# Kernel optimization log

Hardware: AMD Instinct MI355X
Metric: run time of the kernel (lower is better)

## Reference

```python
import jax, jax.numpy as jnp
from jax import lax
import numpy as np

B = 4096

def _conv(x, w, b):
    # x: [B,C,H,W], w: [O,I,3,3] torch OIHW layout, VALID, stride 1
    y = lax.conv_general_dilated(x, w, (1, 1), 'VALID',
                                 dimension_numbers=('NCHW', 'OIHW', 'NCHW'))
    return y + b[None, :, None, None]

def _pool2(x):
    return lax.reduce_window(x, -jnp.inf, lax.max, (1, 1, 2, 2), (1, 1, 2, 2), 'VALID')

def _lin(x, w, b):
    # torch Linear: y = x @ W^T + b, W: [out, in]
    return x @ w.T + b

def setup_inputs() -> dict:
    key = jax.random.key(0)
    ks = jax.random.split(key, 24)
    def w(k, shape, fan_in):
        return (jax.random.normal(k, shape, dtype=jnp.float32) / np.sqrt(fan_in)).astype(jnp.float32)
    inp = {
        'x':      jax.random.normal(ks[0], (B, 1, 28, 28), dtype=jnp.float32),
        'c1_w':   w(ks[1], (50, 1, 3, 3), 9),      'c1_b':  jnp.zeros((50,), jnp.float32),
        'c2_w':   w(ks[2], (50, 50, 3, 3), 450),   'c2_b':  jnp.zeros((50,), jnp.float32),
        'c3_w':   w(ks[3], (50, 50, 3, 3), 450),   'c3_b':  jnp.zeros((50,), jnp.float32),
        'l1c1_w': w(ks[4], (500, 50 * 13 * 13), 50 * 13 * 13), 'l1c1_b': jnp.zeros((500,), jnp.float32),
        'l2c1_w': w(ks[5], (10, 500), 500),        'l2c1_b': jnp.zeros((10,), jnp.float32),
        'l1c2_w': w(ks[6], (500, 50 * 5 * 5), 50 * 5 * 5),     'l1c2_b': jnp.zeros((500,), jnp.float32),
        'l2c2_w': w(ks[7], (10, 500), 500),        'l2c2_b': jnp.zeros((10,), jnp.float32),
        'l1_w':   w(ks[8], (500, 50), 50),         'l1_b':  jnp.zeros((500,), jnp.float32),
        'l2_w':   w(ks[9], (10, 500), 500),        'l2_b':  jnp.zeros((10,), jnp.float32),
        'd1_w':   w(ks[10], (2, 50 * 13 * 13), 50 * 13 * 13),  'd1_b':  jnp.zeros((2,), jnp.float32),
        'd2_w':   w(ks[11], (2, 50 * 5 * 5), 50 * 5 * 5),      'd2_b':  jnp.zeros((2,), jnp.float32),
    }
    return inp

def reference(x, c1_w, c1_b, c2_w, c2_b, c3_w, c3_b,
              l1c1_w, l1c1_b, l2c1_w, l2c1_b,
              l1c2_w, l1c2_b, l2c2_w, l2c2_b,
              l1_w, l1_b, l2_w, l2_b, d1_w, d1_b, d2_w, d2_b):
    b = x.shape[0]
    # stage 1
    h1 = _pool2(jax.nn.relu(_conv(x, c1_w, c1_b)))           # [B,50,13,13]
    f1 = h1.reshape(b, 50 * 13 * 13)
    exit1 = jnp.argmax(_lin(f1, d1_w, d1_b), axis=1) == 0     # [B] bool
    out1 = _lin(_lin(f1, l1c1_w, l1c1_b), l2c1_w, l2c1_b)     # [B,10] (no relu, as in source)
    # stage 2 (computed densely; selection below replicates the gather/scatter routing)
    h2 = _pool2(jax.nn.relu(_conv(h1, c2_w, c2_b)))          # [B,50,5,5]
    f2 = h2.reshape(b, 50 * 5 * 5)
    exit2 = jnp.argmax(_lin(f2, d2_w, d2_b), axis=1) == 0
    out2 = _lin(_lin(f2, l1c2_w, l1c2_b), l2c2_w, l2c2_b)
    # stage 3
    h3 = _pool2(jax.nn.relu(_conv(h2, c3_w, c3_b)))          # [B,50,1,1]
    f3 = h3.reshape(b, 50)
    out3 = _lin(jax.nn.relu(_lin(f3, l1_w, l1_b)), l2_w, l2_b)
    sel = jnp.where(exit1[:, None], out1, jnp.where(exit2[:, None], out2, out3))
    # original returns cat(out1_subset, out2_subset, out3_subset) + an index order;
    # we return the equivalent per-sample outputs in original batch order.
    return jax.nn.log_softmax(sel, axis=1)
```

## Files before the change

### kernel.cpp

```cpp
#include <hip/hip_runtime.h>
#include <hip/hip_bf16.h>
#include <cstdint>


typedef __bf16 bf16_t;
typedef __bf16 bf16x8 __attribute__((ext_vector_type(8)));
typedef float  f32x4  __attribute__((ext_vector_type(4)));

#define B_IMG 4096


__device__ void role_conv1(char* smem, int blk,
    const float* __restrict__ x, const float* __restrict__ w1,
    const float* __restrict__ b1, float* __restrict__ h1)
{
    float* ws = (float*)smem;
    float* bs = ws + 456;
    const int t = threadIdx.x;
    for (int i = t; i < 450; i += 256) ws[i] = w1[i];
    if (t < 50) bs[t] = b1[t];
    __syncthreads();

    const int idx = blk * 256 + t;
    if (idx >= B_IMG * 169) return;
    const int b   = idx / 169;
    const int pos = idx % 169;
    const int py = pos / 13, px = pos % 13;

    const float* xp = x + (size_t)b * 784 + (2 * py) * 28 + 2 * px;
    float p[4][4];
#pragma unroll
    for (int r = 0; r < 4; ++r)
#pragma unroll
        for (int c = 0; c < 4; ++c) p[r][c] = xp[r * 28 + c];

    float* hb = h1 + (size_t)b * 8480 + pos;
    if (pos < 30) h1[(size_t)b * 8480 + 8450 + pos] = 0.f;

    for (int oc = 0; oc < 50; ++oc) {
        const float* wp = &ws[oc * 9];
        const float w00 = wp[0], w01 = wp[1], w02 = wp[2];
        const float w10 = wp[3], w11 = wp[4], w12 = wp[5];
        const float w20 = wp[6], w21 = wp[7], w22 = wp[8];
        float a[2][2];
#pragma unroll
        for (int dy = 0; dy < 2; ++dy)
#pragma unroll
            for (int dx = 0; dx < 2; ++dx) {
                a[dy][dx] = p[dy + 0][dx + 0] * w00 + p[dy + 0][dx + 1] * w01 + p[dy + 0][dx + 2] * w02
                          + p[dy + 1][dx + 0] * w10 + p[dy + 1][dx + 1] * w11 + p[dy + 1][dx + 2] * w12
                          + p[dy + 2][dx + 0] * w20 + p[dy + 2][dx + 1] * w21 + p[dy + 2][dx + 2] * w22;
            }
        float v = fmaxf(fmaxf(a[0][0], a[0][1]), fmaxf(a[1][0], a[1][1])) + bs[oc];
        hb[oc * 169] = fmaxf(v, 0.f);
    }
}

__device__ void role_wb16(int blk, const float* __restrict__ src,
                          bf16_t* __restrict__ dst, int N, int K, int Kp, int total)
{
    const int idx = blk * 256 + threadIdx.x;
    if (idx >= total) return;
    const int n = idx / Kp, k = idx % Kp;
    const float v = (n < N && k < K) ? src[(size_t)n * K + k] : 0.f;
    dst[idx] = (bf16_t)v;
}

__device__ void role_w2t(int blk, const float* __restrict__ w2, float* __restrict__ w2p)
{
    const int idx = blk * 256 + threadIdx.x;
    if (idx >= 50 * 600) return;
    const int ic = idx / 600, r = idx % 600, oc = r / 12, j = r % 12;
    w2p[idx] = (j < 9) ? w2[oc * 450 + ic * 9 + j] : 0.f;
}

__device__ void role_conv2(char* smem, int b,
    const float* __restrict__ h1, const float* __restrict__ w2p,
    const float* __restrict__ b2, float* __restrict__ h2)
{
    float* in   = (float*)smem;
    float* wbuf = in + 1360;
    const int t = threadIdx.x;

    for (int s = t; s < 676; s += 256) in[s] = h1[(size_t)b * 8480 + s];
    {
        const float4* src = (const float4*)w2p;
        float4* dst = (float4*)wbuf;
        for (int s = t; s < 600; s += 256) dst[s] = src[s];
    }
    __syncthreads();
    if (t < 30) h2[(size_t)b * 1280 + 1250 + t] = 0.f;

    const int ocg = t / 25;
    const int pos = t % 25;
    const int py = pos / 5, px = pos % 5;
    const int oc0 = ocg * 5;
    const bool act = (t < 250);

    float acc[5][4];
#pragma unroll
    for (int j = 0; j < 5; ++j)
#pragma unroll
        for (int q = 0; q < 4; ++q) acc[j][q] = 0.f;

    for (int ic0 = 0; ic0 < 50; ic0 += 4) {
        const int cur = (ic0 >> 2) & 1;
        if (ic0 + 4 < 50) {
            const int nxt = cur ^ 1;
            const int nic2 = (50 - ic0 - 4 < 4) ? (50 - ic0 - 4) : 4;
            for (int s = t; s < nic2 * 169; s += 256)
                in[nxt * 680 + s] = h1[(size_t)b * 8480 + (ic0 + 4) * 169 + s];
            const float4* src = (const float4*)(w2p + (size_t)(ic0 + 4) * 600);
            float4* dst = (float4*)(wbuf + nxt * 2400);
            for (int s = t; s < nic2 * 150; s += 256) dst[s] = src[s];
        }
        if (act) {
            const int nic = (50 - ic0 < 4) ? (50 - ic0) : 4;
            const float* ibc = in + cur * 680 + (2 * py) * 13 + 2 * px;
            for (int icl = 0; icl < nic; ++icl) {
                float p[4][4];
                const float* ip = ibc + icl * 169;
#pragma unroll
                for (int r = 0; r < 4; ++r)
#pragma unroll
                    for (int c = 0; c < 4; ++c) p[r][c] = ip[r * 13 + c];
                const float* wl = wbuf + cur * 2400 + icl * 600 + oc0 * 12;
#pragma unroll
                for (int j = 0; j < 5; ++j) {
                    const f32x4 wv0 = *(const f32x4*)(wl + j * 12);
                    const f32x4 wv1 = *(const f32x4*)(wl + j * 12 + 4);
                    const f32x4 wv2 = *(const f32x4*)(wl + j * 12 + 8);
                    const float w00 = wv0[0], w01 = wv0[1], w02 = wv0[2];
                    const float w10 = wv0[3], w11 = wv1[0], w12 = wv1[1];
                    const float w20 = wv1[2], w21 = wv1[3], w22 = wv2[0];
#pragma unroll
                    for (int dy = 0; dy < 2; ++dy)
#pragma unroll
                        for (int dx = 0; dx < 2; ++dx) {
                            acc[j][dy * 2 + dx] +=
                                  p[dy + 0][dx + 0] * w00 + p[dy + 0][dx + 1] * w01 + p[dy + 0][dx + 2] * w02
                                + p[dy + 1][dx + 0] * w10 + p[dy + 1][dx + 1] * w11 + p[dy + 1][dx + 2] * w12
                                + p[dy + 2][dx + 0] * w20 + p[dy + 2][dx + 1] * w21 + p[dy + 2][dx + 2] * w22;
                        }
                }
            }
        }
        __syncthreads();
    }

    if (act) {
#pragma unroll
        for (int j = 0; j < 5; ++j) {
            float v = fmaxf(fmaxf(acc[j][0], acc[j][1]), fmaxf(acc[j][2], acc[j][3]));
            h2[(size_t)b * 1280 + (oc0 + j) * 25 + pos] = fmaxf(v + b2[oc0 + j], 0.f);
        }
    }
}

__device__ void role_conv3(char* smem, int blk,
    const float* __restrict__ h2, const float* __restrict__ w3,
    const float* __restrict__ b3, float* __restrict__ f3)
{
    float* in = (float*)smem;
    const int t = threadIdx.x;
    for (int i = t; i < 5000; i += 256) {
        const int img = i / 1250, off = i % 1250;
        in[i] = h2[(size_t)(blk * 4 + img) * 1280 + off];
    }
    __syncthreads();
    const int il = t >> 6;
    const int oc = t & 63;
    if (oc >= 50) return;

    const float* ip0 = &in[il * 1250];
    float a00 = 0.f, a01 = 0.f, a10 = 0.f, a11 = 0.f;
    for (int ic = 0; ic < 50; ++ic) {
        float p[4][4];
        const float* ip = ip0 + ic * 25;
#pragma unroll
        for (int r = 0; r < 4; ++r)
#pragma unroll
            for (int c = 0; c < 4; ++c) p[r][c] = ip[r * 5 + c];
        const float* wp = &w3[((size_t)oc * 50 + ic) * 9];
        const float w00 = wp[0], w01 = wp[1], w02 = wp[2];
        const float w10 = wp[3], w11 = wp[4], w12 = wp[5];
        const float w20 = wp[6], w21 = wp[7], w22 = wp[8];
        a00 += p[0][0]*w00 + p[0][1]*w01 + p[0][2]*w02 + p[1][0]*w10 + p[1][1]*w11 + p[1][2]*w12 + p[2][0]*w20 + p[2][1]*w21 + p[2][2]*w22;
        a01 += p[0][1]*w00 + p[0][2]*w01 + p[0][3]*w02 + p[1][1]*w10 + p[1][2]*w11 + p[1][3]*w12 + p[2][1]*w20 + p[2][2]*w21 + p[2][3]*w22;
        a10 += p[1][0]*w00 + p[1][1]*w01 + p[1][2]*w02 + p[2][0]*w10 + p[2][1]*w11 + p[2][2]*w12 + p[3][0]*w20 + p[3][1]*w21 + p[3][2]*w22;
        a11 += p[1][1]*w00 + p[1][2]*w01 + p[1][3]*w02 + p[2][1]*w10 + p[2][2]*w11 + p[2][3]*w12 + p[3][1]*w20 + p[3][2]*w21 + p[3][3]*w22;
    }
    float v = fmaxf(fmaxf(a00, a01), fmaxf(a10, a11)) + b3[oc];
    f3[(size_t)(blk * 4 + il) * 50 + oc] = fmaxf(v, 0.f);
}

__device__ void role_exit(char* smem, int b,
    const float* __restrict__ F, int ldf, int K,
    const float* __restrict__ dw, const float* __restrict__ db, int* __restrict__ e)
{
    float* r0 = (float*)smem;
    float* r1 = r0 + 256;
    const int t = threadIdx.x;
    const float* f = F + (size_t)b * ldf;
    float s0 = 0.f, s1 = 0.f;
    for (int i = t; i < K; i += 256) {
        const float v = f[i];
        s0 += v * dw[i];
        s1 += v * dw[K + i];
    }
    r0[t] = s0; r1[t] = s1;
    __syncthreads();
    for (int s = 128; s > 0; s >>= 1) {
        if (t < s) { r0[t] += r0[t + s]; r1[t] += r1[t + s]; }
        __syncthreads();
    }
    if (t == 0) e[b] = (r0[0] + db[0] >= r1[0] + db[1]) ? 1 : 0;
}

__device__ void role_gemm(char* smem, int g,
    const float* __restrict__ A, int lda, const bf16_t* __restrict__ W,
    const float* __restrict__ bias, float* __restrict__ C0, float* __restrict__ C1,
    int Kp, int khalf, int Nout, int ldc)
{
    bf16_t* As = (bf16_t*)smem;
    bf16_t* Bs = As + 128 * 40;

    const int t = threadIdx.x;
    const int m0 = (g & 31) * 128;
    const int n0 = ((g >> 5) & 7) * 64;
    const int kz = g >> 8;
    const int kbeg = kz ? khalf : 0;
    const int kend = kz ? Kp : khalf;
    float* C = kz ? C1 : C0;

    const int wave = t >> 6;
    const int lane = t & 63;
    const int wm = (wave >> 1) * 64;
    const int wn = (wave & 1) * 32;
    const int quad = lane >> 4;
    const int lr = lane & 15;

    f32x4 acc[4][2];
#pragma unroll
    for (int i = 0; i < 4; ++i)
#pragma unroll
        for (int j = 0; j < 2; ++j) acc[i][j] = (f32x4)0.f;

    const int ar = t >> 2;
    const int ac = (t & 3) * 8;

    for (int k0 = kbeg; k0 < kend; k0 += 32) {
        __syncthreads();
#pragma unroll
        for (int h = 0; h < 2; ++h) {
            const float* ap = A + (size_t)(m0 + ar + h * 64) * lda + k0 + ac;
            const float4 f0 = *(const float4*)ap;
            const float4 f1 = *(const float4*)(ap + 4);
            bf16x8 v;
            v[0] = (bf16_t)f0.x; v[1] = (bf16_t)f0.y; v[2] = (bf16_t)f0.z; v[3] = (bf16_t)f0.w;
            v[4] = (bf16_t)f1.x; v[5] = (bf16_t)f1.y; v[6] = (bf16_t)f1.z; v[7] = (bf16_t)f1.w;
            *(bf16x8*)&As[(ar + h * 64) * 40 + ac] = v;
        }
        *(uint4*)&Bs[ar * 40 + ac] = *(const uint4*)&W[(size_t)(n0 + ar) * Kp + k0 + ac];
        __syncthreads();

        bf16x8 af[4], bfr[2];
#pragma unroll
        for (int i = 0; i < 4; ++i)
            af[i] = *(const bf16x8*)&As[(wm + i * 16 + lr) * 40 + quad * 8];
#pragma unroll
        for (int j = 0; j < 2; ++j)
            bfr[j] = *(const bf16x8*)&Bs[(wn + j * 16 + lr) * 40 + quad * 8];
#pragma unroll
        for (int i = 0; i < 4; ++i)
#pragma unroll
            for (int j = 0; j < 2; ++j)
                acc[i][j] = __builtin_amdgcn_mfma_f32_16x16x32_bf16(af[i], bfr[j], acc[i][j], 0, 0, 0);
    }

#pragma unroll
    for (int j = 0; j < 2; ++j) {
        const int n = n0 + wn + j * 16 + lr;
        const float bv = (kz == 0 && n < Nout) ? bias[n] : 0.f;
#pragma unroll
        for (int i = 0; i < 4; ++i) {
            const int mrow = m0 + wm + i * 16 + quad * 4;
#pragma unroll
            for (int r = 0; r < 4; ++r)
                C[(size_t)(mrow + r) * ldc + n] = acc[i][j][r] + bv;
        }
    }
}

__device__ void role_lin10(char* smem, int blk,
    const float* __restrict__ U, const float* __restrict__ U2, int ldu,
    const float* __restrict__ W, const float* __restrict__ bias,
    float* __restrict__ out)
{
    float* red = (float*)smem;
    const int t = threadIdx.x;
    const int ks = t & 15;
    const int il = t >> 4;
    const int b  = blk * 16 + il;
    const float* u = U + (size_t)b * ldu;

    float acc[10];
#pragma unroll
    for (int o = 0; o < 10; ++o) acc[o] = 0.f;

    if (U2) {
        const float* u2 = U2 + (size_t)b * ldu;
        for (int i = 0; i < 31; ++i) {
            const int k = ks + i * 16;
            const float uv = u[k] + u2[k];
#pragma unroll
            for (int o = 0; o < 10; ++o) acc[o] += uv * W[o * 500 + k];
        }
        const int k = ks + 496;
        if (k < 500) {
            const float uv = u[k] + u2[k];
#pragma unroll
            for (int o = 0; o < 10; ++o) acc[o] += uv * W[o * 500 + k];
        }
    } else {
        for (int i = 0; i < 31; ++i) {
            const int k = ks + i * 16;
            const float uv = u[k];
#pragma unroll
            for (int o = 0; o < 10; ++o) acc[o] += uv * W[o * 500 + k];
        }
        const int k = ks + 496;
        if (k < 500) {
            const float uv = u[k];
#pragma unroll
            for (int o = 0; o < 10; ++o) acc[o] += uv * W[o * 500 + k];
        }
    }
#pragma unroll
    for (int o = 0; o < 10; ++o) red[(il * 10 + o) * 17 + ks] = acc[o];
    __syncthreads();
    if (t < 160) {
        const int il2 = t / 10, o = t - il2 * 10;
        float s = 0.f;
#pragma unroll
        for (int q = 0; q < 16; ++q) s += red[(il2 * 10 + o) * 17 + q];
        out[(size_t)(blk * 16 + il2) * 10 + o] = s + bias[o];
    }
}


__global__ __launch_bounds__(256) void k_prep(
    const float* x, const float* c1w, const float* c1b, float* h1,
    const float* l1c1w, bf16_t* Wb1, const float* l1c2w, bf16_t* Wb2,
    const float* c2w, float* w2p)
{
    extern __shared__ char smem[];
    const int g = blockIdx.x;
    if (g < 2704)        role_conv1(smem, g, x, c1w, c1b, h1);
    else if (g < 19664)  role_wb16(g - 2704, l1c1w, Wb1, 500, 8450, 8480, 512 * 8480);
    else if (g < 22224)  role_wb16(g - 19664, l1c2w, Wb2, 500, 1250, 1280, 512 * 1280);
    else                 role_w2t(g - 22224, c2w, w2p);
}

__global__ __launch_bounds__(256) void k_stage1(
    const float* h1, const bf16_t* Wb1, const float* l1c1b, float* u, float* up,
    const float* d1w, const float* d1b, int* e1,
    const float* w2p, const float* c2b, float* h2)
{
    extern __shared__ char smem[];
    const int g = blockIdx.x;
    if (g < 512)         role_gemm(smem, g, h1, 8480, Wb1, l1c1b, u, up, 8480, 4256, 500, 512);
    else if (g < 4608)   role_conv2(smem, g - 512, h1, w2p, c2b, h2);
    else                 role_exit(smem, g - 4608, h1, 8480, 8450, d1w, d1b, e1);
}

__global__ __launch_bounds__(256) void k_stage2(
    const float* h2, const bf16_t* Wb2, const float* l1c2b, float* v, float* vp,
    const float* d2w, const float* d2b, int* e2,
    const float* c3w, const float* c3b, float* f3,
    const float* u, const float* up, const float* l2c1w, const float* l2c1b, float* out1)
{
    extern __shared__ char smem[];
    const int g = blockIdx.x;
    if (g < 512)         role_gemm(smem, g, h2, 1280, Wb2, l1c2b, v, vp, 1280, 640, 500, 512);
    else if (g < 1536)   role_conv3(smem, g - 512, h2, c3w, c3b, f3);
    else if (g < 1792)   role_lin10(smem, g - 1536, u, up, 512, l2c1w, l2c1b, out1);
    else                 role_exit(smem, g - 1792, h2, 1280, 1250, d2w, d2b, e2);
}

__global__ __launch_bounds__(256) void k_tail(
    const float* __restrict__ v, const float* __restrict__ vp,
    const float* __restrict__ l2c2w, const float* __restrict__ l2c2b,
    const float* __restrict__ f3, const float* __restrict__ l1w, const float* __restrict__ l1b,
    const float* __restrict__ l2w, const float* __restrict__ l2b,
    const float* __restrict__ out1, const int* __restrict__ e1, const int* __restrict__ e2,
    float* __restrict__ out)
{
    __shared__ float fs[800];
    __shared__ float u3loc[8000];
    __shared__ float red[2720];
    __shared__ float o2loc[160];
    __shared__ float o3loc[160];

    const int t   = threadIdx.x;
    const int blk = blockIdx.x;
    const int ks  = t & 15;
    const int il  = t >> 4;

    for (int i = t; i < 800; i += 256) fs[i] = f3[(size_t)blk * 800 + i];
    __syncthreads();

    for (int im = 0; im < 16; ++im) {
        for (int o = t; o < 500; o += 256) {
            float s = 0.f;
#pragma unroll
            for (int k = 0; k < 50; ++k) s += fs[im * 50 + k] * l1w[o * 50 + k];
            u3loc[im * 500 + o] = fmaxf(s + l1b[o], 0.f);
        }
    }

    {
        const float* uu  = v  + (size_t)(blk * 16 + il) * 512;
        const float* uu2 = vp + (size_t)(blk * 16 + il) * 512;
        float acc[10];
#pragma unroll
        for (int o = 0; o < 10; ++o) acc[o] = 0.f;
        for (int i = 0; i < 31; ++i) {
            const int k = ks + i * 16;
            const float uv = uu[k] + uu2[k];
#pragma unroll
            for (int o = 0; o < 10; ++o) acc[o] += uv * l2c2w[o * 500 + k];
        }
        const int k = ks + 496;
        if (k < 500) {
            const float uv = uu[k] + uu2[k];
#pragma unroll
            for (int o = 0; o < 10; ++o) acc[o] += uv * l2c2w[o * 500 + k];
        }
        __syncthreads();
#pragma unroll
        for (int o = 0; o < 10; ++o) red[(il * 10 + o) * 17 + ks] = acc[o];
        __syncthreads();
        if (t < 160) {
            const int il2 = t / 10, o = t - il2 * 10;
            float s = 0.f;
#pragma unroll
            for (int q = 0; q < 16; ++q) s += red[(il2 * 10 + o) * 17 + q];
            o2loc[t] = s + l2c2b[o];
        }
        __syncthreads();
    }

    {
        const float* uu = u3loc + il * 500;
        float acc[10];
#pragma unroll
        for (int o = 0; o < 10; ++o) acc[o] = 0.f;
        for (int i = 0; i < 31; ++i) {
            const int k = ks + i * 16;
            const float uv = uu[k];
#pragma unroll
            for (int o = 0; o < 10; ++o) acc[o] += uv * l2w[o * 500 + k];
        }
        const int k = ks + 496;
        if (k < 500) {
            const float uv = uu[k];
#pragma unroll
            for (int o = 0; o < 10; ++o) acc[o] += uv * l2w[o * 500 + k];
        }
#pragma unroll
        for (int o = 0; o < 10; ++o) red[(il * 10 + o) * 17 + ks] = acc[o];
        __syncthreads();
        if (t < 160) {
            const int il2 = t / 10, o = t - il2 * 10;
            float s = 0.f;
#pragma unroll
            for (int q = 0; q < 16; ++q) s += red[(il2 * 10 + o) * 17 + q];
            o3loc[t] = s + l2b[o];
        }
        __syncthreads();
    }

    if (t < 16) {
        const int b = blk * 16 + t;
        float vv[10];
        if (e1[b]) {
            const float* src = out1 + (size_t)b * 10;
#pragma unroll
            for (int o = 0; o < 10; ++o) vv[o] = src[o];
        } else if (e2[b]) {
#pragma unroll
            for (int o = 0; o < 10; ++o) vv[o] = o2loc[t * 10 + o];
        } else {
#pragma unroll
            for (int o = 0; o < 10; ++o) vv[o] = o3loc[t * 10 + o];
        }
        float m = -3.4e38f;
#pragma unroll
        for (int o = 0; o < 10; ++o) m = fmaxf(m, vv[o]);
        float s = 0.f;
#pragma unroll
        for (int o = 0; o < 10; ++o) s += expf(vv[o] - m);
        const float ls = logf(s);
#pragma unroll
        for (int o = 0; o < 10; ++o) out[(size_t)b * 10 + o] = vv[o] - m - ls;
    }
}

static inline size_t align256(size_t v) { return (v + 255) & ~(size_t)255; }

extern "C" void kernel_launch(void* const* d_in, const int* in_sizes, int n_in,
                              void* d_out, int out_size, void* d_ws, size_t ws_size,
                              hipStream_t stream)
{
    const float* x     = (const float*)d_in[0];
    const float* c1w   = (const float*)d_in[1];
    const float* c1b   = (const float*)d_in[2];
    const float* c2w   = (const float*)d_in[3];
    const float* c2b   = (const float*)d_in[4];
    const float* c3w   = (const float*)d_in[5];
    const float* c3b   = (const float*)d_in[6];
    const float* l1c1w = (const float*)d_in[7];
    const float* l1c1b = (const float*)d_in[8];
    const float* l2c1w = (const float*)d_in[9];
    const float* l2c1b = (const float*)d_in[10];
    const float* l1c2w = (const float*)d_in[11];
    const float* l1c2b = (const float*)d_in[12];
    const float* l2c2w = (const float*)d_in[13];
    const float* l2c2b = (const float*)d_in[14];
    const float* l1w   = (const float*)d_in[15];
    const float* l1b   = (const float*)d_in[16];
    const float* l2w   = (const float*)d_in[17];
    const float* l2b   = (const float*)d_in[18];
    const float* d1w   = (const float*)d_in[19];
    const float* d1b   = (const float*)d_in[20];
    const float* d2w   = (const float*)d_in[21];
    const float* d2b   = (const float*)d_in[22];

    size_t off = 0;
    const size_t oWb1  = off; off = align256(off + (size_t)512 * 8480 * 2);
    const size_t oWb2  = off; off = align256(off + (size_t)512 * 1280 * 2);
    const size_t oW2P  = off; off = align256(off + (size_t)50 * 600 * 4);
    const size_t oOut1 = off; off = align256(off + (size_t)B_IMG * 10 * 4);
    const size_t oE1   = off; off = align256(off + (size_t)B_IMG * 4);
    const size_t oE2   = off; off = align256(off + (size_t)B_IMG * 4);
    const size_t oH1   = off; off = align256(off + (size_t)B_IMG * 8480 * 4);
    const size_t oH2   = off; off = align256(off + (size_t)B_IMG * 1280 * 4);
    const size_t oU    = off; off = align256(off + (size_t)B_IMG * 512 * 4);
    const size_t oUP   = off; off = align256(off + (size_t)B_IMG * 512 * 4);
    const size_t oF3   = off; off = align256(off + (size_t)B_IMG * 50 * 4);

    char* ws = (char*)d_ws;
    bf16_t* Wb1  = (bf16_t*)(ws + oWb1);
    bf16_t* Wb2  = (bf16_t*)(ws + oWb2);
    float*  w2p  = (float*) (ws + oW2P);
    float*  out1 = (float*) (ws + oOut1);
    int*    e1   = (int*)   (ws + oE1);
    int*    e2   = (int*)   (ws + oE2);
    float*  h1   = (float*) (ws + oH1);
    float*  h2   = (float*) (ws + oH2);
    float*  u    = (float*) (ws + oU);
    float*  up   = (float*) (ws + oUP);
    float*  f3   = (float*) (ws + oF3);
    float*  v    = h1;
    float*  vp   = h1 + (size_t)B_IMG * 512;

    float* out = (float*)d_out;

    k_prep<<<22342, 256, 2048, stream>>>(x, c1w, c1b, h1, l1c1w, Wb1, l1c2w, Wb2, c2w, w2p);
    k_stage1<<<8704, 256, 24832, stream>>>(h1, Wb1, l1c1b, u, up, d1w, d1b, e1, w2p, c2b, h2);
    k_stage2<<<5888, 256, 20000, stream>>>(h2, Wb2, l1c2b, v, vp, d2w, d2b, e2,
                                           c3w, c3b, f3, u, up, l2c1w, l2c1b, out1);
    k_tail<<<256, 256, 0, stream>>>(v, vp, l2c2w, l2c2b, f3, l1w, l1b, l2w, l2b,
                                    out1, e1, e2, out);

    (void)in_sizes; (void)n_in; (void)out_size; (void)ws_size;
}
```

Baseline: 733.5 us.

## Restructure conv2 to two images per block with wave-uniform scalar weight loads

The conv2 role now handles two images per block. Each wave owns 12-13 output channels, and its lanes cover both images' 25 pooled positions. Because the channel range is made wave-uniform via readfirstlane, the weights can be read directly from global memory as scalar loads, which removes the LDS weight staging and the separate weight-transpose prep pass. Each lane holds more accumulators, which raises register pressure and may lower occupancy. Block count, shared-memory use and per-block weight traffic all drop.

New measurement: 883.1 us. +20.4%, slower.

```diff
diff --git a/kernel.cpp b/kernel.cpp
--- a/kernel.cpp
+++ b/kernel.cpp
@@ -66,82 +66,82 @@
     dst[idx] = (bf16_t)v;
 }
 
-__device__ void role_w2t(int blk, const float* __restrict__ w2, float* __restrict__ w2p)
-{
-    const int idx = blk * 256 + threadIdx.x;
-    if (idx >= 50 * 600) return;
-    const int ic = idx / 600, r = idx % 600, oc = r / 12, j = r % 12;
-    w2p[idx] = (j < 9) ? w2[oc * 450 + ic * 9 + j] : 0.f;
-}
-
-__device__ void role_conv2(char* smem, int b,
-    const float* __restrict__ h1, const float* __restrict__ w2p,
+__device__ void role_conv2(char* smem, int blk,
+    const float* __restrict__ h1, const float* __restrict__ w2,
     const float* __restrict__ b2, float* __restrict__ h2)
 {
-    float* in   = (float*)smem;
-    float* wbuf = in + 1360;
-    const int t = threadIdx.x;
-
-    for (int s = t; s < 676; s += 256) in[s] = h1[(size_t)b * 8480 + s];
-    {
-        const float4* src = (const float4*)w2p;
-        float4* dst = (float4*)wbuf;
-        for (int s = t; s < 600; s += 256) dst[s] = src[s];
-    }
+    float* in = (float*)smem;
+    const int t  = threadIdx.x;
+    const int b0 = blk * 2;
+
+#pragma unroll
+    for (int img = 0; img < 2; ++img)
+        for (int s = t; s < 676; s += 256)
+            in[img * 680 + s] = h1[(size_t)(b0 + img) * 8480 + s];
     __syncthreads();
-    if (t < 30) h2[(size_t)b * 1280 + 1250 + t] = 0.f;
-
-    const int ocg = t / 25;
-    const int pos = t % 25;
+    if (t < 60) h2[(size_t)(b0 + t / 30) * 1280 + 1250 + (t % 30)] = 0.f;
+
+    const int lane = t & 63;
+    const int wv   = t >> 6;
+    const int oc0  = __builtin_amdgcn_readfirstlane((wv < 2) ? wv * 13 : 26 + (wv - 2) * 12);
+    const int noc  = __builtin_amdgcn_readfirstlane(13 - (wv >> 1));
+
+    const bool act = (lane < 50);
+    const int img2 = act ? (lane / 25) : 0;
+    const int pos  = act ? (lane % 25) : 0;
     const int py = pos / 5, px = pos % 5;
-    const int oc0 = ocg * 5;
-    const bool act = (t < 250);
-
-    float acc[5][4];
-#pragma unroll
-    for (int j = 0; j < 5; ++j)
+    const int pofs = img2 * 680 + (2 * py) * 13 + 2 * px;
+
+    float acc[13][4];
+#pragma unroll
+    for (int j = 0; j < 13; ++j)
 #pragma unroll
         for (int q = 0; q < 4; ++q) acc[j][q] = 0.f;
 
+#pragma unroll 1
     for (int ic0 = 0; ic0 < 50; ic0 += 4) {
         const int cur = (ic0 >> 2) & 1;
         if (ic0 + 4 < 50) {
             const int nxt = cur ^ 1;
             const int nic2 = (50 - ic0 - 4 < 4) ? (50 - ic0 - 4) : 4;
-            for (int s = t; s < nic2 * 169; s += 256)
-                in[nxt * 680 + s] = h1[(size_t)b * 8480 + (ic0 + 4) * 169 + s];
-            const float4* src = (const float4*)(w2p + (size_t)(ic0 + 4) * 600);
-            float4* dst = (float4*)(wbuf + nxt * 2400);
-            for (int s = t; s < nic2 * 150; s += 256) dst[s] = src[s];
-        }
+#pragma unroll
+            for (int img = 0; img < 2; ++img)
+                for (int s = t; s < nic2 * 169; s += 256)
+                    in[nxt * 1360 + img * 680 + s] =
+                        h1[(size_t)(b0 + img) * 8480 + (ic0 + 4) * 169 + s];
+        }
+        const int nic = (50 - ic0 < 4) ? (50 - ic0) : 4;
         if (act) {
-            const int nic = (50 - ic0 < 4) ? (50 - ic0) : 4;
-            const float* ibc = in + cur * 680 + (2 * py) * 13 + 2 * px;
-            for (int icl = 0; icl < nic; ++icl) {
-                float p[4][4];
-                const float* ip = ibc + icl * 169;
-#pragma unroll
-                for (int r = 0; r < 4; ++r)
-#pragma unroll
-                    for (int c = 0; c < 4; ++c) p[r][c] = ip[r * 13 + c];
-                const float* wl = wbuf + cur * 2400 + icl * 600 + oc0 * 12;
-#pragma unroll
-                for (int j = 0; j < 5; ++j) {
-                    const f32x4 wv0 = *(const f32x4*)(wl + j * 12);
-                    const f32x4 wv1 = *(const f32x4*)(wl + j * 12 + 4);
-                    const f32x4 wv2 = *(const f32x4*)(wl + j * 12 + 8);
-                    const float w00 = wv0[0], w01 = wv0[1], w02 = wv0[2];
-                    const float w10 = wv0[3], w11 = wv1[0], w12 = wv1[1];
-                    const float w20 = wv1[2], w21 = wv1[3], w22 = wv2[0];
-#pragma unroll
-                    for (int dy = 0; dy < 2; ++dy)
-#pragma unroll
-                        for (int dx = 0; dx < 2; ++dx) {
-                            acc[j][dy * 2 + dx] +=
-                                  p[dy + 0][dx + 0] * w00 + p[dy + 0][dx + 1] * w01 + p[dy + 0][dx + 2] * w02
-                                + p[dy + 1][dx + 0] * w10 + p[dy + 1][dx + 1] * w11 + p[dy + 1][dx + 2] * w12
-                                + p[dy + 2][dx + 0] * w20 + p[dy + 2][dx + 1] * w21 + p[dy + 2][dx + 2] * w22;
+#pragma unroll
+            for (int icl = 0; icl < 4; ++icl) {
+                if (icl < nic) {
+                    const int ic = ic0 + icl;
+                    const float* ip = in + cur * 1360 + pofs + icl * 169;
+                    float p[4][4];
+#pragma unroll
+                    for (int r = 0; r < 4; ++r)
+#pragma unroll
+                        for (int c = 0; c < 4; ++c) p[r][c] = ip[r * 13 + c];
+
+                    const float* wic = w2 + (size_t)oc0 * 450 + ic * 9;
+#pragma unroll
+                    for (int j = 0; j < 13; ++j) {
+                        if (j < noc) {
+                            const float* wp = wic + j * 450;
+                            const float w00 = wp[0], w01 = wp[1], w02 = wp[2];
+                            const float w10 = wp[3], w11 = wp[4], w12 = wp[5];
+                            const float w20 = wp[6], w21 = wp[7], w22 = wp[8];
+#pragma unroll
+                            for (int dy = 0; dy < 2; ++dy)
+#pragma unroll
+                                for (int dx = 0; dx < 2; ++dx) {
+                                    acc[j][dy * 2 + dx] +=
+                                          p[dy + 0][dx + 0] * w00 + p[dy + 0][dx + 1] * w01 + p[dy + 0][dx + 2] * w02
+                                        + p[dy + 1][dx + 0] * w10 + p[dy + 1][dx + 1] * w11 + p[dy + 1][dx + 2] * w12
+                                        + p[dy + 2][dx + 0] * w20 + p[dy + 2][dx + 1] * w21 + p[dy + 2][dx + 2] * w22;
+                                }
                         }
+                    }
                 }
             }
         }
@@ -150,9 +150,12 @@
 
     if (act) {
 #pragma unroll
-        for (int j = 0; j < 5; ++j) {
-            float v = fmaxf(fmaxf(acc[j][0], acc[j][1]), fmaxf(acc[j][2], acc[j][3]));
-            h2[(size_t)b * 1280 + (oc0 + j) * 25 + pos] = fmaxf(v + b2[oc0 + j], 0.f);
+        for (int j = 0; j < 13; ++j) {
+            if (j < noc) {
+                float v = fmaxf(fmaxf(acc[j][0], acc[j][1]), fmaxf(acc[j][2], acc[j][3]));
+                v = fmaxf(v + b2[oc0 + j], 0.f);
+                h2[(size_t)(b0 + img2) * 1280 + (oc0 + j) * 25 + pos] = v;
+            }
         }
     }
 }
@@ -351,27 +354,25 @@
 
 __global__ __launch_bounds__(256) void k_prep(
     const float* x, const float* c1w, const float* c1b, float* h1,
-    const float* l1c1w, bf16_t* Wb1, const float* l1c2w, bf16_t* Wb2,
-    const float* c2w, float* w2p)
+    const float* l1c1w, bf16_t* Wb1, const float* l1c2w, bf16_t* Wb2)
 {
     extern __shared__ char smem[];
     const int g = blockIdx.x;
     if (g < 2704)        role_conv1(smem, g, x, c1w, c1b, h1);
     else if (g < 19664)  role_wb16(g - 2704, l1c1w, Wb1, 500, 8450, 8480, 512 * 8480);
-    else if (g < 22224)  role_wb16(g - 19664, l1c2w, Wb2, 500, 1250, 1280, 512 * 1280);
-    else                 role_w2t(g - 22224, c2w, w2p);
+    else                 role_wb16(g - 19664, l1c2w, Wb2, 500, 1250, 1280, 512 * 1280);
 }
 
 __global__ __launch_bounds__(256) void k_stage1(
     const float* h1, const bf16_t* Wb1, const float* l1c1b, float* u, float* up,
     const float* d1w, const float* d1b, int* e1,
-    const float* w2p, const float* c2b, float* h2)
+    const float* c2w, const float* c2b, float* h2)
 {
     extern __shared__ char smem[];
     const int g = blockIdx.x;
     if (g < 512)         role_gemm(smem, g, h1, 8480, Wb1, l1c1b, u, up, 8480, 4256, 500, 512);
-    else if (g < 4608)   role_conv2(smem, g - 512, h1, w2p, c2b, h2);
-    else                 role_exit(smem, g - 4608, h1, 8480, 8450, d1w, d1b, e1);
+    else if (g < 2560)   role_conv2(smem, g - 512, h1, c2w, c2b, h2);
+    else                 role_exit(smem, g - 2560, h1, 8480, 8450, d1w, d1b, e1);
 }
 
 __global__ __launch_bounds__(256) void k_stage2(
@@ -540,7 +541,6 @@
     size_t off = 0;
     const size_t oWb1  = off; off = align256(off + (size_t)512 * 8480 * 2);
     const size_t oWb2  = off; off = align256(off + (size_t)512 * 1280 * 2);
-    const size_t oW2P  = off; off = align256(off + (size_t)50 * 600 * 4);
     const size_t oOut1 = off; off = align256(off + (size_t)B_IMG * 10 * 4);
     const size_t oE1   = off; off = align256(off + (size_t)B_IMG * 4);
     const size_t oE2   = off; off = align256(off + (size_t)B_IMG * 4);
@@ -553,7 +553,6 @@
     char* ws = (char*)d_ws;
     bf16_t* Wb1  = (bf16_t*)(ws + oWb1);
     bf16_t* Wb2  = (bf16_t*)(ws + oWb2);
-    float*  w2p  = (float*) (ws + oW2P);
     float*  out1 = (float*) (ws + oOut1);
     int*    e1   = (int*)   (ws + oE1);
     int*    e2   = (int*)   (ws + oE2);
@@ -567,8 +566,8 @@
 
     float* out = (float*)d_out;
 
-    k_prep<<<22342, 256, 2048, stream>>>(x, c1w, c1b, h1, l1c1w, Wb1, l1c2w, Wb2, c2w, w2p);
-    k_stage1<<<8704, 256, 24832, stream>>>(h1, Wb1, l1c1b, u, up, d1w, d1b, e1, w2p, c2b, h2);
+    k_prep<<<22224, 256, 2048, stream>>>(x, c1w, c1b, h1, l1c1w, Wb1, l1c2w, Wb2);
+    k_stage1<<<6656, 256, 15360, stream>>>(h1, Wb1, l1c1b, u, up, d1w, d1b, e1, c2w, c2b, h2);
     k_stage2<<<5888, 256, 20000, stream>>>(h2, Wb2, l1c2b, v, vp, d2w, d2b, e2,
                                            c3w, c3b, f3, u, up, l2c1w, l2c1b, out1);
     k_tail<<<256, 256, 0, stream>>>(v, vp, l2c2w, l2c2b, f3, l1w, l1b, l2w, l2b,
```
